# Kernel optimization log

Hardware: AMD Instinct MI355X
Metric: run time of the kernel (lower is better)

Reference implementation:

```python
import jax, jax.numpy as jnp
import numpy as np

B, N, D, V, K = 64, 256, 512, 50257, 100
NORM_TERM = float(np.log(V))        # norm_term='auto' -> log(vocab)
BACKOFF_PROB = 1e-10


def setup_inputs() -> dict:
    key = jax.random.key(0)
    k1, k2, k3, k4, k5 = jax.random.split(key, 5)
    inp = jax.random.normal(k1, (B, N, D), jnp.float32)
    emb_weight = jax.random.normal(k2, (V, D), jnp.float32) * 0.02
    emb_bias = jnp.zeros((V,), jnp.float32)
    # noise distribution buffer: probs clamped + renormed, then log (as in __init__)
    freqs = jax.random.uniform(k3, (V,), jnp.float32, 1e-3, 1.0)
    probs = freqs / freqs.sum()
    probs = jnp.clip(probs, BACKOFF_PROB)
    logprob_noise = jnp.log(probs / probs.sum())
    target = jax.random.randint(k4, (B, N), 0, V)
    # alias.draw(1,1,K).expand(B,N,K): a single shared set of K noise samples
    noise_samples = jax.random.randint(k5, (K,), 0, V)
    return {
        "input": inp,
        "emb_weight": emb_weight,
        "emb_bias": emb_bias,
        "logprob_noise": logprob_noise,
        "target": target,
        "noise_samples": noise_samples,
    }


def reference(input, emb_weight, emb_bias, logprob_noise, target, noise_samples):
    k = noise_samples.shape[0]
    # logits under the noise distribution (pure gathers)
    logit_target_in_noise = logprob_noise[target]          # (B, N)
    logit_noise_in_noise = logprob_noise[noise_samples]    # (K,)
    # model scores: gathered embedding rows dotted with hidden states
    tgt_emb = emb_weight[target]                           # (B, N, D)
    logit_target_in_model = (
        jnp.einsum("bnd,bnd->bn", input, tgt_emb) + emb_bias[target] - NORM_TERM
    )                                                      # (B, N)
    noise_emb = emb_weight[noise_samples]                  # (K, D)
    logit_noise_in_model = (
        jnp.einsum("bnd,kd->bnk", input, noise_emb)
        + emb_bias[noise_samples][None, None, :]
        - NORM_TERM
    )                                                      # (B, N, K)
    # NCE: p_true = exp(lm) / (exp(lm) + K*exp(ln)) = sigmoid(lm - ln - log K)
    # BCE with label [1, 0, ..., 0]:
    #   -loss = log_sigmoid(x) at target slot, log_sigmoid(-x) at noise slots
    log_k = jnp.log(jnp.asarray(k, dtype=input.dtype))
    x_t = logit_target_in_model - logit_target_in_noise - log_k             # (B, N)
    x_n = logit_noise_in_model - logit_noise_in_noise[None, None, :] - log_k  # (B, N, K)
    per_pos = jax.nn.log_sigmoid(x_t) + jnp.sum(jax.nn.log_sigmoid(-x_n), axis=2)
    return jnp.sum(per_pos, axis=1)  # (B,)
```

## Files before the change

kernel.cpp:

```cpp
#include <hip/hip_runtime.h>
#include <math.h>

#define Dq 512
#define Vq 50257
#define Kq 100
#define KP 112
#define NORM_TERM 10.8249051f
#define LOGK 4.6051702f
#define NBLK 1024
#define DT_STRIDE 3584

typedef __attribute__((ext_vector_type(8))) short short8;
typedef __attribute__((ext_vector_type(4))) float floatx4;
typedef __attribute__((ext_vector_type(4))) unsigned short ushort4v;
typedef __attribute__((ext_vector_type(8))) unsigned short ushort8v;

__device__ __forceinline__ unsigned short f2bf(float f) {
    union { float f; unsigned u; } v; v.f = f;
    unsigned r = v.u + 0x7FFFu + ((v.u >> 16) & 1u);
    return (unsigned short)(r >> 16);
}

__device__ __forceinline__ short8 cvt8(floatx4 a, floatx4 b) {
    short8 o;
    o[0] = (short)f2bf(a.x); o[1] = (short)f2bf(a.y);
    o[2] = (short)f2bf(a.z); o[3] = (short)f2bf(a.w);
    o[4] = (short)f2bf(b.x); o[5] = (short)f2bf(b.y);
    o[6] = (short)f2bf(b.z); o[7] = (short)f2bf(b.w);
    return o;
}

__device__ __forceinline__ float dot4(floatx4 a, floatx4 b) {
    return a.x*b.x + a.y*b.y + a.z*b.z + a.w*b.w;
}

__device__ __forceinline__ float log_sigmoid(float x) {
    return fminf(x, 0.f) - __logf(1.f + __expf(-fabsf(x)));
}

__global__ void prep_noise(const float* __restrict__ emb_w,
                           const float* __restrict__ emb_b,
                           const float* __restrict__ lpn,
                           const int* __restrict__ ns,
                           unsigned short* __restrict__ nBT,
                           float* __restrict__ nAdj) {
    int k = blockIdx.x;
    int t = threadIdx.x;
    size_t off = (size_t)(t >> 3) * DT_STRIDE + k * 32 + (t & 7) * 4;
    if (k < Kq) {
        int row = ns[k];
        floatx4 v = ((const floatx4*)(emb_w + (size_t)row * Dq))[t];
        ushort4v o;
        o.x = f2bf(v.x); o.y = f2bf(v.y); o.z = f2bf(v.z); o.w = f2bf(v.w);
        *(ushort4v*)(nBT + off) = o;
        if (t == 0) nAdj[k] = emb_b[row] - NORM_TERM - lpn[row] - LOGK;
    } else {
        ushort4v z; z.x = 0; z.y = 0; z.z = 0; z.w = 0;
        *(ushort4v*)(nBT + off) = z;
        if (t == 0) nAdj[k] = 0.f;
    }
}

__global__ __launch_bounds__(256, 4) void nce_main(
    const float* __restrict__ input,
    const float* __restrict__ emb_w,
    const float* __restrict__ emb_b,
    const float* __restrict__ lpn,
    const int* __restrict__ target,
    const unsigned short* __restrict__ nBT,
    const float* __restrict__ nAdj,
    float* __restrict__ partials)
{
    __shared__ unsigned short A_lds[16 * 512];
    __shared__ float tdot[16];

    int tid  = threadIdx.x;
    int lane = tid & 63;
    int w    = tid >> 6;
    int pos0 = (int)blockIdx.x * 16;
    int r16  = lane & 15;
    int g4   = lane >> 4;

#pragma unroll
    for (int j = 0; j < 4; ++j) {
        int row = w * 4 + j;
        const float* src = input + (size_t)(pos0 + row) * Dq + lane * 8;
        int tg = target[pos0 + row];
        const float* tsrc = emb_w + (size_t)tg * Dq + lane * 8;
        floatx4 x0 = *(const floatx4*)(src);
        floatx4 x1 = *(const floatx4*)(src + 4);
        floatx4 t0 = *(const floatx4*)(tsrc);
        floatx4 t1 = *(const floatx4*)(tsrc + 4);
        float s = dot4(x0, t0) + dot4(x1, t1);
#pragma unroll
        for (int off = 32; off >= 1; off >>= 1)
            s += __shfl_xor(s, off);
        if (lane == 0) tdot[row] = s;
        char* base = (char*)A_lds + row * 1024;
        *(ushort8v*)(base + ((lane * 16) ^ ((row & 7) << 4))) = (ushort8v)cvt8(x0, x1);
    }
    __syncthreads();

    const char* abase = (const char*)A_lds + r16 * 1024;
    int asw = (r16 & 7) << 4;

    float contrib = 0.f;

    if (w < 3) {
        const unsigned short* p0 = nBT + (size_t)(2 * w) * 512 + r16 * 32 + g4 * 8;
        floatx4 acc0 = {0.f, 0.f, 0.f, 0.f};
        floatx4 acc1 = {0.f, 0.f, 0.f, 0.f};
#pragma unroll
        for (int dt = 0; dt < 16; ++dt) {
            short8 a  = *(const short8*)(abase + ((dt * 64 + g4 * 16) ^ asw));
            short8 f0 = *(const short8*)(p0 + (size_t)dt * DT_STRIDE);
            short8 f1 = *(const short8*)(p0 + (size_t)dt * DT_STRIDE + 512);
            acc0 = __builtin_amdgcn_mfma_f32_16x16x32_bf16(a, f0, acc0, 0, 0, 0);
            acc1 = __builtin_amdgcn_mfma_f32_16x16x32_bf16(a, f1, acc1, 0, 0, 0);
        }
        float adj0 = nAdj[w * 32 + r16];
        float adj1 = nAdj[w * 32 + 16 + r16];
#pragma unroll
        for (int r = 0; r < 4; ++r) {
            contrib += log_sigmoid(-(acc0[r] + adj0));
            contrib += log_sigmoid(-(acc1[r] + adj1));
        }
    } else {
        const unsigned short* p6 = nBT + (size_t)6 * 512 + r16 * 32 + g4 * 8;
        floatx4 acc6 = {0.f, 0.f, 0.f, 0.f};
#pragma unroll
        for (int dt = 0; dt < 16; ++dt) {
            short8 a  = *(const short8*)(abase + ((dt * 64 + g4 * 16) ^ asw));
            short8 f6 = *(const short8*)(p6 + (size_t)dt * DT_STRIDE);
            acc6 = __builtin_amdgcn_mfma_f32_16x16x32_bf16(a, f6, acc6, 0, 0, 0);
        }
        if (96 + r16 < Kq) {
            float adj6 = nAdj[96 + r16];
#pragma unroll
            for (int r = 0; r < 4; ++r)
                contrib += log_sigmoid(-(acc6[r] + adj6));
        }
        if (g4 == 0) {
            int tg = target[pos0 + r16];
            float xt = tdot[r16] + emb_b[tg] - NORM_TERM - lpn[tg] - LOGK;
            contrib += log_sigmoid(xt);
        }
    }

#pragma unroll
    for (int off = 32; off >= 1; off >>= 1)
        contrib += __shfl_xor(contrib, off);
    if (lane == 0) partials[(size_t)blockIdx.x * 4 + w] = contrib;
}

__global__ void finalize(const float* __restrict__ partials,
                         float* __restrict__ out) {
    __shared__ float s4[64][5];
    int t = threadIdx.x;
    int b = t >> 2, q = t & 3;
    float s = 0.f;
#pragma unroll
    for (int i = 0; i < 16; ++i) s += partials[b * 64 + q * 16 + i];
    s4[b][q] = s;
    __syncthreads();
    if (t < 64) out[t] = s4[t][0] + s4[t][1] + s4[t][2] + s4[t][3];
}

extern "C" void kernel_launch(void* const* d_in, const int* in_sizes, int n_in,
                              void* d_out, int out_size, void* d_ws, size_t ws_size,
                              hipStream_t stream) {
    const float* input = (const float*)d_in[0];
    const float* emb_w = (const float*)d_in[1];
    const float* emb_b = (const float*)d_in[2];
    const float* lpn   = (const float*)d_in[3];
    const int*   tgt   = (const int*)d_in[4];
    const int*   ns    = (const int*)d_in[5];
    float* out = (float*)d_out;

    unsigned short* nBT = (unsigned short*)d_ws;
    float* nAdj     = (float*)((char*)d_ws + (size_t)KP * Dq * 2);
    float* partials = (float*)((char*)d_ws + (size_t)KP * Dq * 2 + 512);

    prep_noise<<<KP, 128, 0, stream>>>(emb_w, emb_b, lpn, ns, nBT, nAdj);
    nce_main<<<NBLK, 256, 0, stream>>>(input, emb_w, emb_b, lpn, tgt, nBT, nAdj,
                                       partials);
    finalize<<<1, 256, 0, stream>>>(partials, out);
}
```

Before: 28.95 us.

## Process 32 positions per block with 8 waves sharing each noise B-fragment

Each block now handles 32 positions with 512 threads. Seven waves each own one 16-column noise tile and apply it to two 16-row A tiles, so every noise fragment loaded from global memory feeds two MFMAs. The eighth wave computes only the target terms. This halves the block count and the number of global noise-fragment loads, in exchange for doubled LDS use per block and an idle wave during the MMA phase. Partials still total 4096 and finalize is unchanged.

```diff
diff --git a/kernel.cpp b/kernel.cpp
--- a/kernel.cpp
+++ b/kernel.cpp
@@ -7,7 +7,7 @@
 #define KP 112
 #define NORM_TERM 10.8249051f
 #define LOGK 4.6051702f
-#define NBLK 1024
+#define NBLK 512
 #define DT_STRIDE 3584
 
 typedef __attribute__((ext_vector_type(8))) short short8;
@@ -61,7 +61,7 @@
     }
 }
 
-__global__ __launch_bounds__(256, 4) void nce_main(
+__global__ __launch_bounds__(512, 4) void nce_main(
     const float* __restrict__ input,
     const float* __restrict__ emb_w,
     const float* __restrict__ emb_b,
@@ -71,13 +71,13 @@
     const float* __restrict__ nAdj,
     float* __restrict__ partials)
 {
-    __shared__ unsigned short A_lds[16 * 512];
-    __shared__ float tdot[16];
+    __shared__ unsigned short A_lds[32 * 512];
+    __shared__ float tdot[32];
 
     int tid  = threadIdx.x;
     int lane = tid & 63;
     int w    = tid >> 6;
-    int pos0 = (int)blockIdx.x * 16;
+    int pos0 = (int)blockIdx.x * 32;
     int r16  = lane & 15;
     int g4   = lane >> 4;
 
@@ -101,48 +101,38 @@
     }
     __syncthreads();
 
-    const char* abase = (const char*)A_lds + r16 * 1024;
-    int asw = (r16 & 7) << 4;
-
     float contrib = 0.f;
 
-    if (w < 3) {
-        const unsigned short* p0 = nBT + (size_t)(2 * w) * 512 + r16 * 32 + g4 * 8;
+    if (w < 7) {
+        const char* a0base = (const char*)A_lds + r16 * 1024;
+        const char* a1base = a0base + 16 * 1024;
+        int asw = (r16 & 7) << 4;
+        const unsigned short* p = nBT + (size_t)w * 512 + r16 * 32 + g4 * 8;
         floatx4 acc0 = {0.f, 0.f, 0.f, 0.f};
         floatx4 acc1 = {0.f, 0.f, 0.f, 0.f};
 #pragma unroll
         for (int dt = 0; dt < 16; ++dt) {
-            short8 a  = *(const short8*)(abase + ((dt * 64 + g4 * 16) ^ asw));
-            short8 f0 = *(const short8*)(p0 + (size_t)dt * DT_STRIDE);
-            short8 f1 = *(const short8*)(p0 + (size_t)dt * DT_STRIDE + 512);
-            acc0 = __builtin_amdgcn_mfma_f32_16x16x32_bf16(a, f0, acc0, 0, 0, 0);
-            acc1 = __builtin_amdgcn_mfma_f32_16x16x32_bf16(a, f1, acc1, 0, 0, 0);
+            int aoff = (dt * 64 + g4 * 16) ^ asw;
+            short8 a0 = *(const short8*)(a0base + aoff);
+            short8 a1 = *(const short8*)(a1base + aoff);
+            short8 f  = *(const short8*)(p + (size_t)dt * DT_STRIDE);
+            acc0 = __builtin_amdgcn_mfma_f32_16x16x32_bf16(a0, f, acc0, 0, 0, 0);
+            acc1 = __builtin_amdgcn_mfma_f32_16x16x32_bf16(a1, f, acc1, 0, 0, 0);
         }
-        float adj0 = nAdj[w * 32 + r16];
-        float adj1 = nAdj[w * 32 + 16 + r16];
+        int k = w * 16 + r16;
+        if (k < Kq) {
+            float adj = nAdj[k];
 #pragma unroll
-        for (int r = 0; r < 4; ++r) {
-            contrib += log_sigmoid(-(acc0[r] + adj0));
-            contrib += log_sigmoid(-(acc1[r] + adj1));
+            for (int r = 0; r < 4; ++r) {
+                contrib += log_sigmoid(-(acc0[r] + adj));
+                contrib += log_sigmoid(-(acc1[r] + adj));
+            }
         }
     } else {
-        const unsigned short* p6 = nBT + (size_t)6 * 512 + r16 * 32 + g4 * 8;
-        floatx4 acc6 = {0.f, 0.f, 0.f, 0.f};
-#pragma unroll
-        for (int dt = 0; dt < 16; ++dt) {
-            short8 a  = *(const short8*)(abase + ((dt * 64 + g4 * 16) ^ asw));
-            short8 f6 = *(const short8*)(p6 + (size_t)dt * DT_STRIDE);
-            acc6 = __builtin_amdgcn_mfma_f32_16x16x32_bf16(a, f6, acc6, 0, 0, 0);
-        }
-        if (96 + r16 < Kq) {
-            float adj6 = nAdj[96 + r16];
-#pragma unroll
-            for (int r = 0; r < 4; ++r)
-                contrib += log_sigmoid(-(acc6[r] + adj6));
-        }
-        if (g4 == 0) {
-            int tg = target[pos0 + r16];
-            float xt = tdot[r16] + emb_b[tg] - NORM_TERM - lpn[tg] - LOGK;
+        if (g4 < 2) {
+            int p32 = g4 * 16 + r16;
+            int tg = target[pos0 + p32];
+            float xt = tdot[p32] + emb_b[tg] - NORM_TERM - lpn[tg] - LOGK;
             contrib += log_sigmoid(xt);
         }
     }
@@ -150,7 +140,7 @@
 #pragma unroll
     for (int off = 32; off >= 1; off >>= 1)
         contrib += __shfl_xor(contrib, off);
-    if (lane == 0) partials[(size_t)blockIdx.x * 4 + w] = contrib;
+    if (lane == 0) partials[(size_t)blockIdx.x * 8 + w] = contrib;
 }
 
 __global__ void finalize(const float* __restrict__ partials,
@@ -182,7 +172,7 @@
     float* partials = (float*)((char*)d_ws + (size_t)KP * Dq * 2 + 512);
 
     prep_noise<<<KP, 128, 0, stream>>>(emb_w, emb_b, lpn, ns, nBT, nAdj);
-    nce_main<<<NBLK, 256, 0, stream>>>(input, emb_w, emb_b, lpn, tgt, nBT, nAdj,
+    nce_main<<<NBLK, 512, 0, stream>>>(input, emb_w, emb_b, lpn, tgt, nBT, nAdj,
                                        partials);
     finalize<<<1, 256, 0, stream>>>(partials, out);
 }
```

Result: faster. 27.28 us (-5.8%).
